# Kernel tuning notes

Measured on AMD Instinct MI355X. Metric: run time of the kernel, lower is better.

Reference implementation:

```python
import jax, jax.numpy as jnp
import numpy as np

C = 4          # number of low-frequency rFFT coefficients kept
EPS = 1e-12    # LayerNorm eps


def setup_inputs() -> dict:
    key = jax.random.key(0)
    k1, k2 = jax.random.split(key)
    B, S, H = 16, 2048, 1024
    input_tensor = jax.random.normal(k1, (B, S, H), dtype=jnp.float32)
    sqrt_beta = jax.random.normal(k2, (1, 1, H), dtype=jnp.float32)
    ln_gamma = jnp.ones((H,), dtype=jnp.float32)
    ln_beta = jnp.zeros((H,), dtype=jnp.float32)
    return {
        "input_tensor": input_tensor,
        "sqrt_beta": sqrt_beta,
        "ln_gamma": ln_gamma,
        "ln_beta": ln_beta,
    }


def _layer_norm(x, gamma, beta):
    mean = jnp.mean(x, axis=-1, keepdims=True)
    var = jnp.mean((x - mean) ** 2, axis=-1, keepdims=True)  # biased, like torch
    return (x - mean) * jax.lax.rsqrt(var + EPS) * gamma + beta


def reference(input_tensor, sqrt_beta, ln_gamma, ln_beta):
    B, S, H = input_tensor.shape
    x = jnp.fft.rfft(input_tensor, axis=1, norm="ortho")  # [B, S//2+1, H] complex
    freq = jnp.arange(x.shape[1])[None, :, None]
    low = jnp.where(freq < C, x, 0.0)                      # zero all coeffs >= c
    low_pass = jnp.fft.irfft(low, n=S, axis=1, norm="ortho")
    high_pass = input_tensor - low_pass
    seq_emb_fft = low_pass + (sqrt_beta ** 2) * high_pass
    # Dropout(0.5) treated as identity (eval mode) for a deterministic reference.
    return _layer_norm(seq_emb_fft + input_tensor, ln_gamma, ln_beta)
```

## Files before the change

kernel.cpp:

```cpp
#include <hip/hip_runtime.h>


constexpr int Sc = 2048;
constexpr int Hc = 1024;
constexpr float TWO_PI_OVER_S = 6.283185307179586f / (float)Sc;

typedef float nfloat4 __attribute__((ext_vector_type(4)));

__device__ __forceinline__ void sincos7(int s, float w[7]) {
    float sn1, cs1;
    sincosf(TWO_PI_OVER_S * (float)s, &sn1, &cs1);
    const float cs2 = fmaf(2.f * cs1, cs1, -1.f);
    const float sn2 = 2.f * sn1 * cs1;
    const float cs3 = cs1 * cs2 - sn1 * sn2;
    const float sn3 = sn1 * cs2 + cs1 * sn2;
    w[0] = 1.f; w[1] = cs1; w[2] = sn1; w[3] = cs2; w[4] = sn2; w[5] = cs3; w[6] = sn3;
}

__global__ __launch_bounds__(256) void freq_coeff_partial(
    const float* __restrict__ x, float* __restrict__ coefp,
    int B, int schunk) {
    const int tid   = threadIdx.x;
    const int b     = blockIdx.y;
    const int chunk = blockIdx.x;
    const int s0    = chunk * schunk;

    const float4* __restrict__ xb =
        reinterpret_cast<const float4*>(x) + (size_t)b * Sc * (Hc / 4) + tid;

    float acc[7][4];
#pragma unroll
    for (int j = 0; j < 7; ++j)
#pragma unroll
        for (int e = 0; e < 4; ++e) acc[j][e] = 0.f;

    for (int si = 0; si < schunk; si += 4) {
        float4 v[4];
#pragma unroll
        for (int r = 0; r < 4; ++r)
            v[r] = xb[(size_t)(s0 + si + r) * (Hc / 4)];
#pragma unroll
        for (int r = 0; r < 4; ++r) {
            float w[7];
            sincos7(s0 + si + r, w);
            const float vv[4] = {v[r].x, v[r].y, v[r].z, v[r].w};
#pragma unroll
            for (int j = 0; j < 7; ++j)
#pragma unroll
                for (int e = 0; e < 4; ++e)
                    acc[j][e] = fmaf(w[j], vv[e], acc[j][e]);
        }
    }

    float4* cp = reinterpret_cast<float4*>(coefp) +
                 ((size_t)chunk * B + b) * 7 * (Hc / 4) + tid;
#pragma unroll
    for (int j = 0; j < 7; ++j) {
        float4 o = {acc[j][0], acc[j][1], acc[j][2], acc[j][3]};
        cp[(size_t)j * (Hc / 4)] = o;
    }
}

__global__ __launch_bounds__(256) void coeff_reduce(
    const float* __restrict__ coefp, float* __restrict__ coef,
    int CK, int n4) {
    const int i = blockIdx.x * 256 + threadIdx.x;
    if (i >= n4) return;
    const float4* __restrict__ p = reinterpret_cast<const float4*>(coefp) + i;
    float4 s = {0.f, 0.f, 0.f, 0.f};
    for (int c = 0; c < CK; ++c) {
        const float4 v = p[(size_t)c * n4];
        s.x += v.x; s.y += v.y; s.z += v.z; s.w += v.w;
    }
    reinterpret_cast<float4*>(coef)[i] = s;
}

__global__ __launch_bounds__(256) void freq_ln_kernel(
    const float* __restrict__ x, const float* __restrict__ coef,
    const float* __restrict__ sqb, const float* __restrict__ gamma,
    const float* __restrict__ lbeta, float* __restrict__ out) {
    const int tid = threadIdx.x;
    const int b   = blockIdx.y;
    const int s0  = blockIdx.x * 4;
    const size_t rowBase = ((size_t)b * Sc + s0) * (Hc / 4) + tid;

    const float4 sb4 = reinterpret_cast<const float4*>(sqb)[tid];
    const float4 g4  = reinterpret_cast<const float4*>(gamma)[tid];
    const float4 be4 = reinterpret_cast<const float4*>(lbeta)[tid];
    const float bb[4] = {sb4.x, sb4.y, sb4.z, sb4.w};
    const float gg[4] = {g4.x, g4.y, g4.z, g4.w};
    const float be[4] = {be4.x, be4.y, be4.z, be4.w};
    float ap[4], am[4];
#pragma unroll
    for (int e = 0; e < 4; ++e) {
        const float t = bb[e] * bb[e];
        ap[e] = 1.f + t;
        am[e] = (1.f - t) * (1.f / (float)Sc);
    }

    const float4* __restrict__ CF =
        reinterpret_cast<const float4*>(coef) + (size_t)b * 7 * (Hc / 4) + tid;
    float cf[7][4];
#pragma unroll
    for (int j = 0; j < 7; ++j) {
        const float4 t = CF[(size_t)j * (Hc / 4)];
        cf[j][0] = t.x; cf[j][1] = t.y; cf[j][2] = t.z; cf[j][3] = t.w;
    }

    float4 xv[4];
#pragma unroll
    for (int r = 0; r < 4; ++r)
        xv[r] = reinterpret_cast<const float4*>(x)[rowBase + (size_t)r * (Hc / 4)];

    float y[4][4], s1[4], s2[4];
#pragma unroll
    for (int r = 0; r < 4; ++r) {
        float w[7];
        sincos7(s0 + r, w);
#pragma unroll
        for (int j = 1; j < 7; ++j) w[j] *= 2.f;
        const float xx[4] = {xv[r].x, xv[r].y, xv[r].z, xv[r].w};
        s1[r] = 0.f; s2[r] = 0.f;
#pragma unroll
        for (int e = 0; e < 4; ++e) {
            float lp = cf[0][e];
#pragma unroll
            for (int j = 1; j < 7; ++j) lp = fmaf(cf[j][e], w[j], lp);
            const float yy = fmaf(ap[e], xx[e], am[e] * lp);
            y[r][e] = yy;
            s1[r] += yy;
            s2[r] = fmaf(yy, yy, s2[r]);
        }
    }

    const int lane = tid & 63, wv = tid >> 6;
#pragma unroll
    for (int off = 32; off > 0; off >>= 1) {
#pragma unroll
        for (int r = 0; r < 4; ++r) {
            s1[r] += __shfl_down(s1[r], off, 64);
            s2[r] += __shfl_down(s2[r], off, 64);
        }
    }
    __shared__ float sm[4][8];
    if (lane == 0) {
#pragma unroll
        for (int r = 0; r < 4; ++r) { sm[wv][r] = s1[r]; sm[wv][4 + r] = s2[r]; }
    }
    __syncthreads();

#pragma unroll
    for (int r = 0; r < 4; ++r) {
        const float m  = (sm[0][r] + sm[1][r] + sm[2][r] + sm[3][r]) * (1.f / (float)Hc);
        const float q  = (sm[0][4 + r] + sm[1][4 + r] + sm[2][4 + r] + sm[3][4 + r]) * (1.f / (float)Hc);
        const float inv = rsqrtf(fmaf(-m, m, q) + 1e-12f);
        nfloat4 o;
        o.x = fmaf((y[r][0] - m) * inv, gg[0], be[0]);
        o.y = fmaf((y[r][1] - m) * inv, gg[1], be[1]);
        o.z = fmaf((y[r][2] - m) * inv, gg[2], be[2]);
        o.w = fmaf((y[r][3] - m) * inv, gg[3], be[3]);
        __builtin_nontemporal_store(o, reinterpret_cast<nfloat4*>(out) + rowBase + (size_t)r * (Hc / 4));
    }
}

extern "C" void kernel_launch(void* const* d_in, const int* in_sizes, int n_in,
                              void* d_out, int out_size, void* d_ws, size_t ws_size,
                              hipStream_t stream) {
    const float* x     = (const float*)d_in[0];
    const float* sqb   = (const float*)d_in[1];
    const float* gamma = (const float*)d_in[2];
    const float* lbeta = (const float*)d_in[3];
    float* out = (float*)d_out;

    const int B = in_sizes[0] / (Sc * Hc);
    const size_t coefElems = (size_t)B * 7 * Hc;
    const size_t coefBytes = coefElems * sizeof(float);

    int CK = 64;
    while (CK > 1 && (size_t)(CK + 1) * coefBytes > ws_size) CK >>= 1;

    float* coefp = (float*)d_ws;
    float* coef  = (CK == 1) ? coefp : coefp + CK * coefElems;

    const int schunk = Sc / CK;
    dim3 g1(CK, B);
    freq_coeff_partial<<<g1, 256, 0, stream>>>(x, coefp, B, schunk);

    if (CK > 1) {
        const int n4 = (int)(coefElems / 4);
        coeff_reduce<<<(n4 + 255) / 256, 256, 0, stream>>>(coefp, coef, CK, n4);
    }

    dim3 g2(Sc / 4, B);
    freq_ln_kernel<<<g2, 256, 0, stream>>>(x, coef, sqb, gamma, lbeta, out);
}
```

Before: 276.5 us.

## Fuse coefficient, reduce, and LayerNorm stages into one cooperative persistent kernel

Replaces the three-kernel pipeline with a single cooperative kernel that computes partial low-frequency coefficients, reduces them, and applies the filter plus LayerNorm, separated by grid-wide syncs. Blocks are persistent and walk contiguous row groups, so each block reloads coefficients only when the batch changes, and the 1/S and 2x scaling is folded into those coefficients once. This removes kernel launch gaps and per-block coefficient reloads. In exchange it adds grid sync overhead and limits parallelism to the co-resident block count (1024 blocks cap), and falls back to the old path if cooperative launch is unavailable.

```diff
diff --git a/kernel.cpp b/kernel.cpp
--- a/kernel.cpp
+++ b/kernel.cpp
@@ -1,8 +1,14 @@
 #include <hip/hip_runtime.h>
+#include <hip/hip_cooperative_groups.h>
+
+namespace cg = cooperative_groups;
 
 
 constexpr int Sc = 2048;
 constexpr int Hc = 1024;
+constexpr int H4 = Hc / 4;
+constexpr int CKc = 64;
+constexpr int SCHUNK = Sc / CKc;
 constexpr float TWO_PI_OVER_S = 6.283185307179586f / (float)Sc;
 
 typedef float nfloat4 __attribute__((ext_vector_type(4)));
@@ -17,6 +23,180 @@
     w[0] = 1.f; w[1] = cs1; w[2] = sn1; w[3] = cs2; w[4] = sn2; w[5] = cs3; w[6] = sn3;
 }
 
+__global__ __launch_bounds__(256, 4) void fused_freq_ln(
+    const float* __restrict__ x, float* __restrict__ coefp,
+    float* __restrict__ coef, const float* __restrict__ sqb,
+    const float* __restrict__ gam, const float* __restrict__ lbeta,
+    float* __restrict__ out, int B)
+{
+    const int tid  = threadIdx.x;
+    const int nblk = gridDim.x;
+    cg::grid_group grid = cg::this_grid();
+
+    const int nTaskA = CKc * B;
+    for (int task = blockIdx.x; task < nTaskA; task += nblk) {
+        const int b     = task / CKc;
+        const int chunk = task - b * CKc;
+        const int s0    = chunk * SCHUNK;
+        const float4* __restrict__ xb =
+            reinterpret_cast<const float4*>(x) + (size_t)b * Sc * H4 + tid;
+
+        float acc[7][4];
+#pragma unroll
+        for (int j = 0; j < 7; ++j)
+#pragma unroll
+            for (int e = 0; e < 4; ++e) acc[j][e] = 0.f;
+
+#pragma unroll 2
+        for (int si = 0; si < SCHUNK; si += 4) {
+            float4 v[4];
+#pragma unroll
+            for (int r = 0; r < 4; ++r)
+                v[r] = xb[(size_t)(s0 + si + r) * H4];
+#pragma unroll
+            for (int r = 0; r < 4; ++r) {
+                float w[7];
+                sincos7(s0 + si + r, w);
+                const float vv[4] = {v[r].x, v[r].y, v[r].z, v[r].w};
+#pragma unroll
+                for (int j = 0; j < 7; ++j)
+#pragma unroll
+                    for (int e = 0; e < 4; ++e)
+                        acc[j][e] = fmaf(w[j], vv[e], acc[j][e]);
+            }
+        }
+
+        float4* cp = reinterpret_cast<float4*>(coefp) +
+                     ((size_t)chunk * B + b) * 7 * H4 + tid;
+#pragma unroll
+        for (int j = 0; j < 7; ++j) {
+            float4 o = {acc[j][0], acc[j][1], acc[j][2], acc[j][3]};
+            cp[(size_t)j * H4] = o;
+        }
+    }
+
+    grid.sync();
+
+    const int n4 = B * 7 * H4;
+    for (int i = blockIdx.x * 256 + tid; i < n4; i += nblk * 256) {
+        const float4* __restrict__ p = reinterpret_cast<const float4*>(coefp) + i;
+        float sx = 0.f, sy = 0.f, sz = 0.f, sw = 0.f;
+#pragma unroll 8
+        for (int c = 0; c < CKc; ++c) {
+            const float4 v = p[(size_t)c * n4];
+            sx += v.x; sy += v.y; sz += v.z; sw += v.w;
+        }
+        const float4 o = {sx, sy, sz, sw};
+        reinterpret_cast<float4*>(coef)[i] = o;
+    }
+
+    grid.sync();
+
+    const float4 sb4 = reinterpret_cast<const float4*>(sqb)[tid];
+    const float4 g4  = reinterpret_cast<const float4*>(gam)[tid];
+    const float4 be4 = reinterpret_cast<const float4*>(lbeta)[tid];
+    const float gg[4] = {g4.x, g4.y, g4.z, g4.w};
+    const float be[4] = {be4.x, be4.y, be4.z, be4.w};
+    float ap[4], am[4];
+    {
+        const float bbv[4] = {sb4.x, sb4.y, sb4.z, sb4.w};
+#pragma unroll
+        for (int e = 0; e < 4; ++e) {
+            const float t = bbv[e] * bbv[e];
+            ap[e] = 1.f + t;
+            am[e] = (1.f - t) * (1.f / (float)Sc);
+        }
+    }
+
+    __shared__ float smred[2][4][8];
+    const int lane = tid & 63, wv = tid >> 6;
+
+    const int nGroup = B * (Sc / 4);
+    const int tpb  = (nGroup + nblk - 1) / nblk;
+    const int gBeg = blockIdx.x * tpb;
+    int gEnd = gBeg + tpb;
+    if (gEnd > nGroup) gEnd = nGroup;
+
+    int curb = -1;
+    float cfx[7][4];
+    int par = 0;
+    for (int g = gBeg; g < gEnd; ++g, par ^= 1) {
+        const int b  = g >> 9;
+        const int s0 = (g & 511) << 2;
+        if (b != curb) {
+            curb = b;
+            const float4* __restrict__ CF =
+                reinterpret_cast<const float4*>(coef) + (size_t)b * 7 * H4 + tid;
+#pragma unroll
+            for (int j = 0; j < 7; ++j) {
+                const float4 t = CF[(size_t)j * H4];
+                const float sc = (j == 0) ? 1.f : 2.f;
+                cfx[j][0] = t.x * am[0] * sc;
+                cfx[j][1] = t.y * am[1] * sc;
+                cfx[j][2] = t.z * am[2] * sc;
+                cfx[j][3] = t.w * am[3] * sc;
+            }
+        }
+
+        const size_t rowBase = ((size_t)b * Sc + s0) * H4 + tid;
+        float4 xv[4];
+#pragma unroll
+        for (int r = 0; r < 4; ++r)
+            xv[r] = reinterpret_cast<const float4*>(x)[rowBase + (size_t)r * H4];
+
+        float y[4][4], s1[4], s2[4];
+#pragma unroll
+        for (int r = 0; r < 4; ++r) {
+            float w[7];
+            sincos7(s0 + r, w);
+            const float xx[4] = {xv[r].x, xv[r].y, xv[r].z, xv[r].w};
+            s1[r] = 0.f; s2[r] = 0.f;
+#pragma unroll
+            for (int e = 0; e < 4; ++e) {
+                float lp = cfx[0][e];
+#pragma unroll
+                for (int j = 1; j < 7; ++j) lp = fmaf(cfx[j][e], w[j], lp);
+                const float yy = fmaf(ap[e], xx[e], lp);
+                y[r][e] = yy;
+                s1[r] += yy;
+                s2[r] = fmaf(yy, yy, s2[r]);
+            }
+        }
+
+#pragma unroll
+        for (int off = 32; off > 0; off >>= 1) {
+#pragma unroll
+            for (int r = 0; r < 4; ++r) {
+                s1[r] += __shfl_down(s1[r], off, 64);
+                s2[r] += __shfl_down(s2[r], off, 64);
+            }
+        }
+        if (lane == 0) {
+#pragma unroll
+            for (int r = 0; r < 4; ++r) {
+                smred[par][wv][r]     = s1[r];
+                smred[par][wv][4 + r] = s2[r];
+            }
+        }
+        __syncthreads();
+
+#pragma unroll
+        for (int r = 0; r < 4; ++r) {
+            const float m = (smred[par][0][r] + smred[par][1][r] +
+                             smred[par][2][r] + smred[par][3][r]) * (1.f / (float)Hc);
+            const float q = (smred[par][0][4+r] + smred[par][1][4+r] +
+                             smred[par][2][4+r] + smred[par][3][4+r]) * (1.f / (float)Hc);
+            const float inv = rsqrtf(fmaf(-m, m, q) + 1e-12f);
+            nfloat4 o;
+            o.x = fmaf((y[r][0] - m) * inv, gg[0], be[0]);
+            o.y = fmaf((y[r][1] - m) * inv, gg[1], be[1]);
+            o.z = fmaf((y[r][2] - m) * inv, gg[2], be[2]);
+            o.w = fmaf((y[r][3] - m) * inv, gg[3], be[3]);
+            __builtin_nontemporal_store(o, reinterpret_cast<nfloat4*>(out) + rowBase + (size_t)r * H4);
+        }
+    }
+}
+
 __global__ __launch_bounds__(256) void freq_coeff_partial(
     const float* __restrict__ x, float* __restrict__ coefp,
     int B, int schunk) {
@@ -26,7 +206,7 @@
     const int s0    = chunk * schunk;
 
     const float4* __restrict__ xb =
-        reinterpret_cast<const float4*>(x) + (size_t)b * Sc * (Hc / 4) + tid;
+        reinterpret_cast<const float4*>(x) + (size_t)b * Sc * H4 + tid;
 
     float acc[7][4];
 #pragma unroll
@@ -38,7 +218,7 @@
         float4 v[4];
 #pragma unroll
         for (int r = 0; r < 4; ++r)
-            v[r] = xb[(size_t)(s0 + si + r) * (Hc / 4)];
+            v[r] = xb[(size_t)(s0 + si + r) * H4];
 #pragma unroll
         for (int r = 0; r < 4; ++r) {
             float w[7];
@@ -53,11 +233,11 @@
     }
 
     float4* cp = reinterpret_cast<float4*>(coefp) +
-                 ((size_t)chunk * B + b) * 7 * (Hc / 4) + tid;
+                 ((size_t)chunk * B + b) * 7 * H4 + tid;
 #pragma unroll
     for (int j = 0; j < 7; ++j) {
         float4 o = {acc[j][0], acc[j][1], acc[j][2], acc[j][3]};
-        cp[(size_t)j * (Hc / 4)] = o;
+        cp[(size_t)j * H4] = o;
     }
 }
 
@@ -82,7 +262,7 @@
     const int tid = threadIdx.x;
     const int b   = blockIdx.y;
     const int s0  = blockIdx.x * 4;
-    const size_t rowBase = ((size_t)b * Sc + s0) * (Hc / 4) + tid;
+    const size_t rowBase = ((size_t)b * Sc + s0) * H4 + tid;
 
     const float4 sb4 = reinterpret_cast<const float4*>(sqb)[tid];
     const float4 g4  = reinterpret_cast<const float4*>(gamma)[tid];
@@ -99,18 +279,18 @@
     }
 
     const float4* __restrict__ CF =
-        reinterpret_cast<const float4*>(coef) + (size_t)b * 7 * (Hc / 4) + tid;
+        reinterpret_cast<const float4*>(coef) + (size_t)b * 7 * H4 + tid;
     float cf[7][4];
 #pragma unroll
     for (int j = 0; j < 7; ++j) {
-        const float4 t = CF[(size_t)j * (Hc / 4)];
+        const float4 t = CF[(size_t)j * H4];
         cf[j][0] = t.x; cf[j][1] = t.y; cf[j][2] = t.z; cf[j][3] = t.w;
     }
 
     float4 xv[4];
 #pragma unroll
     for (int r = 0; r < 4; ++r)
-        xv[r] = reinterpret_cast<const float4*>(x)[rowBase + (size_t)r * (Hc / 4)];
+        xv[r] = reinterpret_cast<const float4*>(x)[rowBase + (size_t)r * H4];
 
     float y[4][4], s1[4], s2[4];
 #pragma unroll
@@ -159,7 +339,7 @@
         o.y = fmaf((y[r][1] - m) * inv, gg[1], be[1]);
         o.z = fmaf((y[r][2] - m) * inv, gg[2], be[2]);
         o.w = fmaf((y[r][3] - m) * inv, gg[3], be[3]);
-        __builtin_nontemporal_store(o, reinterpret_cast<nfloat4*>(out) + rowBase + (size_t)r * (Hc / 4));
+        __builtin_nontemporal_store(o, reinterpret_cast<nfloat4*>(out) + rowBase + (size_t)r * H4);
     }
 }
 
@@ -176,6 +356,31 @@
     const size_t coefElems = (size_t)B * 7 * Hc;
     const size_t coefBytes = coefElems * sizeof(float);
 
+    static int coopMax = -2;
+    if (coopMax == -2) {
+        int dev = 0, nCU = 0, coop = 0, occ = 0;
+        (void)hipGetDevice(&dev);
+        (void)hipDeviceGetAttribute(&nCU, hipDeviceAttributeMultiprocessorCount, dev);
+        (void)hipDeviceGetAttribute(&coop, hipDeviceAttributeCooperativeLaunch, dev);
+        hipError_t oe = hipOccupancyMaxActiveBlocksPerMultiprocessor(
+            &occ, fused_freq_ln, 256, 0);
+        coopMax = (coop && oe == hipSuccess && occ > 0 && nCU > 0) ? occ * nCU : -1;
+    }
+
+    if (coopMax > 0 && (size_t)(CKc + 1) * coefBytes <= ws_size) {
+        float* coefp = (float*)d_ws;
+        float* coef  = coefp + (size_t)CKc * coefElems;
+        int grid = CKc * B;
+        if (grid > coopMax) grid = coopMax;
+        void* args[] = {(void*)&x, (void*)&coefp, (void*)&coef, (void*)&sqb,
+                        (void*)&gamma, (void*)&lbeta, (void*)&out, (void*)&B};
+        hipError_t e = hipLaunchCooperativeKernel((const void*)fused_freq_ln,
+                                                  dim3(grid), dim3(256),
+                                                  args, 0, stream);
+        if (e == hipSuccess) return;
+        (void)hipGetLastError();
+    }
+
     int CK = 64;
     while (CK > 1 && (size_t)(CK + 1) * coefBytes > ws_size) CK >>= 1;
 
```

After: 389.5 us. 1.41x slower.
